# Performance work log

Hardware: AMD Instinct MI355X
Metric: run time of the kernel (lower is better)

## Reference

```python
import jax, jax.numpy as jnp
import numpy as np
from jax import lax

B, L, DDYN, DSTAT, H = 512, 64, 16, 8, 512
N_BANK, C_CAND, K_TOP, N_PROTO = 50000, 1024, 16, 8
T_TARG, Q_QUANT = 2, 3
TEMP = 0.2


def _l2norm(x, eps=1e-12):
    # matches torch.nn.functional.normalize: x / max(||x||, eps)
    n = jnp.sqrt(jnp.sum(x * x, axis=-1, keepdims=True))
    return x / jnp.maximum(n, eps)


def setup_inputs() -> dict:
    key = jax.random.key(0)
    ks = jax.random.split(key, 24)
    s = 0.02
    inp = {
        'sequence_values': jax.random.normal(ks[0], (B, L, DDYN), jnp.float32),
        'sequence_masks': jnp.ones((B, L), jnp.float32),
        'static_values': jax.random.normal(ks[1], (B, DSTAT), jnp.float32),
        'bank_keys': jax.random.normal(ks[2], (N_BANK, H), jnp.float32),
        'bank_values': jax.random.normal(ks[3], (N_BANK, H), jnp.float32),
        'candidate_indices': jax.random.randint(ks[4], (B, C_CAND), 0, N_BANK, jnp.int64),
        # encoder params (SequenceEncoder stand-in: masked-mean + linear + relu)
        'W_seq': jax.random.normal(ks[5], (DDYN, H), jnp.float32) * s,
        'W_stat': jax.random.normal(ks[6], (DSTAT, H), jnp.float32) * s,
        'b_enc': jnp.zeros((H,), jnp.float32),
        # retrieval / prototype / fusion params
        'W_q': jax.random.normal(ks[7], (H, H), jnp.float32) * s,
        'b_q': jnp.zeros((H,), jnp.float32),
        'prototype_tokens': jax.random.normal(ks[8], (N_PROTO, H), jnp.float32) * 0.02,
        'W_tr': jax.random.normal(ks[9], (2 * H, H), jnp.float32) * s,
        'b_tr': jnp.zeros((H,), jnp.float32),
        'W_gate': jax.random.normal(ks[10], (3 * H, H), jnp.float32) * s,
        'b_gate': jnp.zeros((H,), jnp.float32),
        'W_out': jax.random.normal(ks[11], (H, H), jnp.float32) * s,
        'b_out': jnp.zeros((H,), jnp.float32),
        # per-target heads stacked: [T, H, Q] and [T, H]
        'W_quant': jax.random.normal(ks[12], (T_TARG, H, Q_QUANT), jnp.float32) * s,
        'b_quant': jnp.zeros((T_TARG, Q_QUANT), jnp.float32),
        'W_ev': jax.random.normal(ks[13], (T_TARG, H), jnp.float32) * s,
        'b_ev': jnp.zeros((T_TARG,), jnp.float32),
    }
    return inp


def reference(sequence_values, sequence_masks, static_values, bank_keys, bank_values,
              candidate_indices, W_seq, W_stat, b_enc, W_q, b_q, prototype_tokens,
              W_tr, b_tr, W_gate, b_gate, W_out, b_out, W_quant, b_quant, W_ev, b_ev):
    # --- encoder (masked mean pool + linear + relu stand-in for SequenceEncoder) ---
    m = sequence_masks[..., None]                                   # [B,L,1]
    pooled = (sequence_values * m).sum(1) / jnp.maximum(m.sum(1), 1e-6)
    local_hidden = jax.nn.relu(pooled @ W_seq + static_values @ W_stat + b_enc)  # [B,H]

    # --- normalized query ---
    query = _l2norm(local_hidden @ W_q + b_q)                       # [B,H]

    # --- donor retrieval: gather + dot + topk + softmax + weighted sum ---
    cand_keys = bank_keys[candidate_indices]                        # [B,C,H]
    sim = jnp.einsum('bch,bh->bc', cand_keys, query)                # [B,C]
    top_scores, top_pos = lax.top_k(sim, K_TOP)                     # [B,K]
    weights = jax.nn.softmax(top_scores / max(TEMP, 1e-6), axis=-1)
    sel_idx = jnp.take_along_axis(candidate_indices, top_pos, axis=1)  # [B,K]
    donor_hidden = jnp.einsum('bk,bkh->bh', weights, bank_values[sel_idx])

    # --- prototype attention ---
    protos_n = _l2norm(prototype_tokens)                            # [P,H]
    pw = jax.nn.softmax(query @ protos_n.T, axis=-1)                # [B,P]
    proto_hidden = pw @ prototype_tokens                            # [B,H]

    # --- transfer / gate / fuse (dropout is identity at eval) ---
    transfer = jax.nn.relu(jnp.concatenate([donor_hidden, proto_hidden], -1) @ W_tr + b_tr)
    gate = jax.nn.sigmoid(
        jnp.concatenate([local_hidden, donor_hidden, proto_hidden], -1) @ W_gate + b_gate)
    fused = gate * local_hidden + (1.0 - gate) * transfer
    fused = jax.nn.relu(fused @ W_out + b_out)                      # [B,H]

    # --- heads: sorted quantiles [B,T,Q] and event logits [B,T] ---
    quant = jnp.sort(jnp.einsum('bh,thq->btq', fused, W_quant) + b_quant, axis=-1)
    logit = jnp.einsum('bh,th->bt', fused, W_ev) + b_ev
    return jnp.concatenate([quant.reshape(quant.shape[0], -1), logit], axis=-1)  # [B, T*Q+T]
```

## Files before the change

### kernel.cpp

```cpp
#include <hip/hip_runtime.h>
#include <hip/hip_bf16.h>

typedef __hip_bfloat16 bf16;
typedef float f4v __attribute__((ext_vector_type(4)));
typedef float f2v __attribute__((ext_vector_type(2)));

__device__ __forceinline__ float lo16(unsigned u){ return __uint_as_float(u << 16); }
__device__ __forceinline__ float hi16(unsigned u){ return __uint_as_float(u & 0xffff0000u); }

#define Bn 512
#define Hn 512
#define Cn 1024
#define Kn 16
#define NBANK 50000
#define NIDPAD 50176

__device__ __forceinline__ int clamp_id(int id){
    return (id < 0) ? 0 : ((id >= NBANK) ? (NBANK - 1) : id);
}

#define A_OFF    0
#define B_OFF    262144
#define C_OFF    524288
#define D_OFF    786432
#define SIM_OFF  1048576
#define ELO_OFF  1048576
#define EHI_OFF  1310720
#define F_OFF    1572864
#define G_OFF2   1835008
#define WS_FLOATS 2097152

#define HIST_I   0
#define CURSOR_I NIDPAD
#define GTOT_I   (2*NIDPAD)
#define OFFS_I   (2*NIDPAD + 256)

__global__ __launch_bounds__(256) void k_enc(
    const float* __restrict__ seq, const float* __restrict__ mask, const float* __restrict__ stat,
    const float* __restrict__ W_seq, const float* __restrict__ W_stat, const float* __restrict__ b_enc,
    const int* __restrict__ cand32, float* __restrict__ ws)
{
    const int b = blockIdx.x, t = threadIdx.x;
    const int h0 = 2*t, h1 = 2*t + 1;

    {
        const int c64 = ((cand32[1] | cand32[3] | cand32[5] | cand32[7]) == 0) ? 1 : 0;
        int* hist = (int*)(ws + F_OFF) + HIST_I;
        #pragma unroll
        for (int u = 0; u < 4; u++) {
            int idx = b*Cn + u*256 + t;
            atomicAdd(&hist[clamp_id(cand32[(size_t)idx << c64])], 1);
        }
    }

    __shared__ float s_pool[16], s_stat[8];
    if (t < 16) {
        float acc = 0.f, ms = 0.f;
        for (int l = 0; l < 64; l++) {
            float m = mask[b*64 + l];
            ms  += m;
            acc += seq[(b*64 + l)*16 + t] * m;
        }
        s_pool[t] = acc / fmaxf(ms, 1e-6f);
    } else if (t < 24) {
        s_stat[t - 16] = stat[b*8 + (t - 16)];
    }
    __syncthreads();
    float a0 = b_enc[h0], a1 = b_enc[h1];
    #pragma unroll
    for (int j = 0; j < 16; j++) {
        float2 wv = *(const float2*)(W_seq + j*Hn + h0);
        a0 += s_pool[j]*wv.x; a1 += s_pool[j]*wv.y;
    }
    #pragma unroll
    for (int j = 0; j < 8; j++) {
        float2 wv = *(const float2*)(W_stat + j*Hn + h0);
        a0 += s_stat[j]*wv.x; a1 += s_stat[j]*wv.y;
    }
    float* g = ws + B_OFF + (size_t)b*Hn;
    g[h0] = fmaxf(a0, 0.f); g[h1] = fmaxf(a1, 0.f);
}

__global__ __launch_bounds__(256) void k_scan(
    const int* __restrict__ hist, int* __restrict__ offs, int* __restrict__ gtot)
{
    __shared__ int s[256]; __shared__ int sbase;
    const int t = threadIdx.x, g = blockIdx.x*256 + t;
    const int v = hist[g];
    s[t] = v; __syncthreads();
    #pragma unroll
    for (int off = 1; off < 256; off <<= 1) {
        int x = (t >= off) ? s[t - off] : 0;
        __syncthreads();
        s[t] += x;
        __syncthreads();
    }
    if (t == 255) sbase = atomicAdd(gtot, s[255]);
    __syncthreads();
    offs[g] = sbase + s[t] - v;
}

__global__ __launch_bounds__(256) void k_scatter(
    const int* __restrict__ cand32, int* __restrict__ cursor,
    const int* __restrict__ offs, unsigned* __restrict__ refs)
{
    const int i = blockIdx.x*256 + threadIdx.x;
    const int c64 = ((cand32[1] | cand32[3] | cand32[5] | cand32[7]) == 0) ? 1 : 0;
    const int id = clamp_id(cand32[(size_t)i << c64]);
    const int pos = atomicAdd(&cursor[id], 1);
    refs[offs[id] + pos] = (unsigned)i;
}

__global__ __launch_bounds__(256) void k_qgemm_p(
    const float* __restrict__ W, const float* __restrict__ bias,
    const float* __restrict__ in,
    float* __restrict__ P0, float* __restrict__ P1,
    float* __restrict__ P2, float* __restrict__ P3)
{
    const int ct = blockIdx.x, rt = blockIdx.y, kz = blockIdx.z, t = threadIdx.x;
    __shared__ float lt[64][132];
    {
        int r = t >> 2, c0 = (t & 3)*32;
        const float* src = in + (size_t)(rt*64 + r)*Hn + kz*128 + c0;
        #pragma unroll
        for (int i = 0; i < 8; i++)
            *(float4*)&lt[r][c0 + i*4] = *(const float4*)(src + i*4);
    }
    __syncthreads();
    const int col0 = ct*64 + (t & 15)*4, rbase = (t >> 4)*4;
    float acc[4][4];
    if (kz == 0) {
        float4 bv = *(const float4*)(bias + col0);
        #pragma unroll
        for (int i = 0; i < 4; i++) { acc[i][0]=bv.x; acc[i][1]=bv.y; acc[i][2]=bv.z; acc[i][3]=bv.w; }
    } else {
        #pragma unroll
        for (int i = 0; i < 4; i++) { acc[i][0]=0; acc[i][1]=0; acc[i][2]=0; acc[i][3]=0; }
    }
    const float* wp = W + (size_t)(kz*128)*Hn + col0;
    #pragma unroll 4
    for (int k = 0; k < 128; k++) {
        float4 wv = *(const float4*)(wp + (size_t)k*Hn);
        #pragma unroll
        for (int i = 0; i < 4; i++) {
            float a = lt[rbase + i][k];
            acc[i][0] += a*wv.x; acc[i][1] += a*wv.y; acc[i][2] += a*wv.z; acc[i][3] += a*wv.w;
        }
    }
    float* outp = (kz == 0) ? P0 : (kz == 1) ? P1 : (kz == 2) ? P2 : P3;
    #pragma unroll
    for (int i = 0; i < 4; i++) {
        float* op = outp + (size_t)(rt*64 + rbase + i)*Hn + col0;
        *(float4*)op = make_float4(acc[i][0], acc[i][1], acc[i][2], acc[i][3]);
    }
}

__global__ __launch_bounds__(256) void k_qnorm(float* __restrict__ ws)
{
    const int b = blockIdx.x*4 + (threadIdx.x >> 6), lane = threadIdx.x & 63;
    const size_t o = (size_t)b*Hn + lane*8;
    const float* p0 = ws + A_OFF   + o;
    const float* p1 = ws + ELO_OFF + o;
    const float* p2 = ws + EHI_OFF + o;
    const float* p3 = ws + G_OFF2  + o;
    float4 qa, qb;
    {
        float4 a0 = *(const float4*)p0, a1 = *(const float4*)p1,
               a2 = *(const float4*)p2, a3 = *(const float4*)p3;
        qa = make_float4(((a0.x+a1.x)+a2.x)+a3.x, ((a0.y+a1.y)+a2.y)+a3.y,
                         ((a0.z+a1.z)+a2.z)+a3.z, ((a0.w+a1.w)+a2.w)+a3.w);
        float4 b0 = *(const float4*)(p0+4), b1 = *(const float4*)(p1+4),
               b2 = *(const float4*)(p2+4), b3 = *(const float4*)(p3+4);
        qb = make_float4(((b0.x+b1.x)+b2.x)+b3.x, ((b0.y+b1.y)+b2.y)+b3.y,
                         ((b0.z+b1.z)+b2.z)+b3.z, ((b0.w+b1.w)+b2.w)+b3.w);
    }
    float ss = qa.x*qa.x + qa.y*qa.y + qa.z*qa.z + qa.w*qa.w
             + qb.x*qb.x + qb.y*qb.y + qb.z*qb.z + qb.w*qb.w;
    #pragma unroll
    for (int o2 = 32; o2; o2 >>= 1) ss += __shfl_xor(ss, o2);
    float inv = 1.f / fmaxf(sqrtf(ss), 1e-12f);
    qa.x *= inv; qa.y *= inv; qa.z *= inv; qa.w *= inv;
    qb.x *= inv; qb.y *= inv; qb.z *= inv; qb.w *= inv;
    float* qr = ws + A_OFF + o;
    *(float4*)qr = qa; *(float4*)(qr + 4) = qb;
}

#define DI_LOAD(R0,R1,R2,R3,A0,Bq0,A1,Bq1,A2,Bq2,A3,Bq3,BASE) do {                       \
    int j0_=(BASE), j1_=(BASE)+1, j2_=(BASE)+2, j3_=(BASE)+3;                            \
    const int m_ = n - 1;                                                                \
    const int c1_ = (j1_ < n), c2_ = (j2_ < n), c3_ = (j3_ < n);                         \
    j0_ = j0_>m_?m_:j0_; j1_ = j1_>m_?m_:j1_; j2_ = j2_>m_?m_:j2_; j3_ = j3_>m_?m_:j3_;  \
    R0 = (j0_<64)?(unsigned)__shfl((int)refv,j0_):__builtin_nontemporal_load(refs+start+j0_); \
    R1 = (j1_<64)?(unsigned)__shfl((int)refv,j1_):__builtin_nontemporal_load(refs+start+j1_); \
    R2 = (j2_<64)?(unsigned)__shfl((int)refv,j2_):__builtin_nontemporal_load(refs+start+j2_); \
    R3 = (j3_<64)?(unsigned)__shfl((int)refv,j3_):__builtin_nontemporal_load(refs+start+j3_); \
    {   const float* q0_ = qbase + (size_t)(R0>>10)*Hn + lane*8;                         \
        A0 = *(const float4*)q0_; Bq0 = *(const float4*)(q0_+4); }                       \
    if (c1_) { const float* q1_ = qbase + (size_t)(R1>>10)*Hn + lane*8;                  \
        A1 = *(const float4*)q1_; Bq1 = *(const float4*)(q1_+4); }                       \
    if (c2_) { const float* q2_ = qbase + (size_t)(R2>>10)*Hn + lane*8;                  \
        A2 = *(const float4*)q2_; Bq2 = *(const float4*)(q2_+4); }                       \
    if (c3_) { const float* q3_ = qbase + (size_t)(R3>>10)*Hn + lane*8;                  \
        A3 = *(const float4*)q3_; Bq3 = *(const float4*)(q3_+4); }                       \
} while(0)

#define DI_COMP(R0,R1,R2,R3,A0,Bq0,A1,Bq1,A2,Bq2,A3,Bq3,BASE) do {                       \
    float s0_ = ka.x*A0.x + ka.y*A0.y + ka.z*A0.z + ka.w*A0.w                            \
              + kb.x*Bq0.x + kb.y*Bq0.y + kb.z*Bq0.z + kb.w*Bq0.w;                       \
    float s1_ = ka.x*A1.x + ka.y*A1.y + ka.z*A1.z + ka.w*A1.w                            \
              + kb.x*Bq1.x + kb.y*Bq1.y + kb.z*Bq1.z + kb.w*Bq1.w;                       \
    float s2_ = ka.x*A2.x + ka.y*A2.y + ka.z*A2.z + ka.w*A2.w                            \
              + kb.x*Bq2.x + kb.y*Bq2.y + kb.z*Bq2.z + kb.w*Bq2.w;                       \
    float s3_ = ka.x*A3.x + ka.y*A3.y + ka.z*A3.z + ka.w*A3.w                            \
              + kb.x*Bq3.x + kb.y*Bq3.y + kb.z*Bq3.z + kb.w*Bq3.w;                       \
    s0_ += __shfl_xor(s0_,32); s1_ += __shfl_xor(s1_,32);                                \
    s2_ += __shfl_xor(s2_,32); s3_ += __shfl_xor(s3_,32);                                \
    s0_ += __shfl_xor(s0_,16); s1_ += __shfl_xor(s1_,16);                                \
    s2_ += __shfl_xor(s2_,16); s3_ += __shfl_xor(s3_,16);                                \
    s0_ += __shfl_xor(s0_, 8); s1_ += __shfl_xor(s1_, 8);                                \
    s2_ += __shfl_xor(s2_, 8); s3_ += __shfl_xor(s3_, 8);                                \
    int d_ = (lane >> 3) & 3;                                                            \
    float t_ = d_==0 ? s0_ : d_==1 ? s1_ : d_==2 ? s2_ : s3_;                            \
    t_ += __shfl_xor(t_, 4); t_ += __shfl_xor(t_, 2); t_ += __shfl_xor(t_, 1);           \
    if ((lane & 7) == 0 && lane < 32) {                                                  \
        int dd_ = lane >> 3;                                                             \
        if ((BASE) + dd_ < n) {                                                          \
            unsigned rs_ = dd_==0 ? R0 : dd_==1 ? R1 : dd_==2 ? R2 : R3;                 \
            simw[rs_] = t_;                                                              \
        }                                                                                \
    }                                                                                    \
} while(0)

__global__ __launch_bounds__(256) void k_dotinv(
    const float* __restrict__ bank_keys, const unsigned* __restrict__ refs,
    const int* __restrict__ offs, const int* __restrict__ cnt,
    float* __restrict__ ws)
{
    const int id = blockIdx.x*4 + (threadIdx.x >> 6);
    const int lane = threadIdx.x & 63;
    const int n = cnt[id];
    if (n <= 0) return;
    const int start = offs[id];

    const float* kp = bank_keys + (size_t)id*Hn + lane*8;
    f4v kav = __builtin_nontemporal_load((const f4v*)kp);
    f4v kbv = __builtin_nontemporal_load((const f4v*)(kp + 4));
    float4 ka = make_float4(kav.x, kav.y, kav.z, kav.w);
    float4 kb = make_float4(kbv.x, kbv.y, kbv.z, kbv.w);
    const unsigned refv = refs[start + (lane < n ? lane : n - 1)];
    const float* qbase = ws + A_OFF;
    float* simw = ws + SIM_OFF;

    unsigned Ar0,Ar1,Ar2,Ar3, Br0=0,Br1=0,Br2=0,Br3=0;
    float4 Aa0,Ab0,Aa1,Ab1,Aa2,Ab2,Aa3,Ab3;
    float4 Ba0,Bb0,Ba1,Bb1,Ba2,Bb2,Ba3,Bb3;
    Aa0=Ab0=Aa1=Ab1=Aa2=Ab2=Aa3=Ab3=make_float4(0.f,0.f,0.f,0.f);
    Ba0=Bb0=Ba1=Bb1=Ba2=Bb2=Ba3=Bb3=make_float4(0.f,0.f,0.f,0.f);

    DI_LOAD(Ar0,Ar1,Ar2,Ar3, Aa0,Ab0,Aa1,Ab1,Aa2,Ab2,Aa3,Ab3, 0);
    for (int base = 0; ; ) {
        if (base + 4 < n) DI_LOAD(Br0,Br1,Br2,Br3, Ba0,Bb0,Ba1,Bb1,Ba2,Bb2,Ba3,Bb3, base + 4);
        DI_COMP(Ar0,Ar1,Ar2,Ar3, Aa0,Ab0,Aa1,Ab1,Aa2,Ab2,Aa3,Ab3, base);
        if (base + 8 < n) DI_LOAD(Ar0,Ar1,Ar2,Ar3, Aa0,Ab0,Aa1,Ab1,Aa2,Ab2,Aa3,Ab3, base + 8);
        DI_COMP(Br0,Br1,Br2,Br3, Ba0,Bb0,Ba1,Bb1,Ba2,Bb2,Ba3,Bb3, base + 4);
        base += 8;
        if (base >= n) break;
    }
}

__global__ __launch_bounds__(256) void k_select(
    const float* __restrict__ bank_values, const int* __restrict__ cand32,
    const float* __restrict__ proto, float* __restrict__ ws)
{
    const int b = blockIdx.x, t = threadIdx.x;
    const int w = t >> 6, lane = t & 63;
    const int h0 = 2*t, h1 = 2*t + 1;
    const int c64 = ((cand32[1] | cand32[3] | cand32[5] | cand32[7]) == 0) ? 1 : 0;

    __shared__ __align__(16) float s_sim[Cn];
    __shared__ float s_bv[4]; __shared__ int s_bi[4];
    __shared__ float s_topv[Kn]; __shared__ int s_sel[Kn];
    __shared__ float s_w[Kn];
    __shared__ float s_score[8], s_pw[8];

    *(float4*)&s_sim[t*4] = *(const float4*)(ws + SIM_OFF + (size_t)b*Cn + t*4);

    const float* qr = ws + A_OFF + (size_t)b*Hn + lane*8;
    float4 qa = *(const float4*)qr, qb = *(const float4*)(qr + 4);
    float qv[8] = {qa.x, qa.y, qa.z, qa.w, qb.x, qb.y, qb.z, qb.w};
    __syncthreads();

    for (int k = 0; k < Kn; k++) {
        float best = -1e30f; int bi = 0x7fffffff;
        for (int i = t; i < Cn; i += 256) {
            float v = s_sim[i];
            if (v > best || (v == best && i < bi)) { best = v; bi = i; }
        }
        #pragma unroll
        for (int o = 32; o; o >>= 1) {
            float ov = __shfl_xor(best, o); int oi = __shfl_xor(bi, o);
            if (ov > best || (ov == best && oi < bi)) { best = ov; bi = oi; }
        }
        if (lane == 0) { s_bv[w] = best; s_bi[w] = bi; }
        __syncthreads();
        if (t == 0) {
            float bv = s_bv[0]; int bbi = s_bi[0];
            for (int x = 1; x < 4; x++)
                if (s_bv[x] > bv || (s_bv[x] == bv && s_bi[x] < bbi)) { bv = s_bv[x]; bbi = s_bi[x]; }
            if (bbi < 0 || bbi >= Cn) bbi = 0;
            s_topv[k] = bv; s_sel[k] = bbi; s_sim[bbi] = -1e30f;
        }
        __syncthreads();
    }

    if (t == 0) {
        float m = s_topv[0];
        float e[Kn], ssum = 0.f;
        for (int k = 0; k < Kn; k++) { e[k] = __expf((s_topv[k] - m) * 5.0f); ssum += e[k]; }
        float inv = 1.f / ssum;
        for (int k = 0; k < Kn; k++) s_w[k] = e[k] * inv;
    }
    for (int p = w; p < 8; p += 4) {
        const float* pp = proto + (size_t)p*Hn + lane*8;
        float4 pa = *(const float4*)pp, pb = *(const float4*)(pp + 4);
        float f[8] = {pa.x, pa.y, pa.z, pa.w, pb.x, pb.y, pb.z, pb.w};
        float dq = 0.f, sq = 0.f;
        #pragma unroll
        for (int i = 0; i < 8; i++) { dq += f[i]*qv[i]; sq += f[i]*f[i]; }
        #pragma unroll
        for (int o = 32; o; o >>= 1) { dq += __shfl_xor(dq, o); sq += __shfl_xor(sq, o); }
        if (lane == 0) s_score[p] = dq / fmaxf(sqrtf(sq), 1e-12f);
    }
    __syncthreads();
    if (t == 0) {
        float m = s_score[0];
        for (int p = 1; p < 8; p++) m = fmaxf(m, s_score[p]);
        float e[8], ssum = 0.f;
        for (int p = 0; p < 8; p++) { e[p] = __expf(s_score[p] - m); ssum += e[p]; }
        float inv = 1.f / ssum;
        for (int p = 0; p < 8; p++) s_pw[p] = e[p] * inv;
    }
    __syncthreads();

    {
        float a0 = 0.f, a1 = 0.f;
        #pragma unroll
        for (int k = 0; k < Kn; k++) {
            int id = clamp_id(cand32[(size_t)(b*Cn + s_sel[k]) << c64]);
            f2v v = __builtin_nontemporal_load((const f2v*)(bank_values + (size_t)id*Hn + h0));
            a0 += s_w[k]*v.x; a1 += s_w[k]*v.y;
        }
        float* gd = ws + C_OFF + (size_t)b*Hn;
        gd[h0] = a0; gd[h1] = a1;
    }
    {
        float a0 = 0.f, a1 = 0.f;
        #pragma unroll
        for (int p = 0; p < 8; p++) {
            float2 v = *(const float2*)(proto + (size_t)p*Hn + h0);
            a0 += s_pw[p]*v.x; a1 += s_pw[p]*v.y;
        }
        float* gp = ws + D_OFF + (size_t)b*Hn;
        gp[h0] = a0; gp[h1] = a1;
    }
}

__global__ __launch_bounds__(256) void k_gatetr_p(
    const float* __restrict__ W_tr, const float* __restrict__ b_tr,
    const float* __restrict__ W_gate, const float* __restrict__ b_gate,
    float* __restrict__ ws)
{
    const int ct = blockIdx.x, rt = blockIdx.y, z = blockIdx.z, t = threadIdx.x;
    const int isGate = (z < 3);
    const int sl = isGate ? z : (z - 3);
    const float* W = isGate ? (W_gate + (size_t)(z*512)*Hn) : (W_tr + (size_t)(sl*512)*Hn);
    const float* slab = ws + B_OFF + (size_t)(isGate ? z : (sl + 1))*262144;
    float* outp = isGate
        ? ((z == 0) ? ws + A_OFF : (z == 1) ? ws + ELO_OFF : ws + EHI_OFF)
        : ((sl == 0) ? ws + F_OFF : ws + G_OFF2);

    __shared__ float lt[32][260];
    const int col0 = ct*128 + (t & 31)*4, rbase = (t >> 5)*4;
    float acc[4][4];
    if (z == 0 || z == 3) {
        const float* bias = isGate ? b_gate : b_tr;
        float4 bv = *(const float4*)(bias + col0);
        #pragma unroll
        for (int i = 0; i < 4; i++) { acc[i][0]=bv.x; acc[i][1]=bv.y; acc[i][2]=bv.z; acc[i][3]=bv.w; }
    } else {
        #pragma unroll
        for (int i = 0; i < 4; i++) { acc[i][0]=0; acc[i][1]=0; acc[i][2]=0; acc[i][3]=0; }
    }

    #pragma unroll
    for (int h = 0; h < 2; h++) {
        if (h) __syncthreads();
        {
            int r = t >> 3, c0 = (t & 7)*32;
            const float* src = slab + (size_t)(rt*32 + r)*Hn + h*256 + c0;
            #pragma unroll
            for (int i = 0; i < 8; i++)
                *(float4*)&lt[r][c0 + i*4] = *(const float4*)(src + i*4);
        }
        __syncthreads();
        const float* wp = W + (size_t)(h*256)*Hn + col0;
        #pragma unroll 4
        for (int k = 0; k < 256; k++) {
            float4 wv = *(const float4*)(wp + (size_t)k*Hn);
            #pragma unroll
            for (int i = 0; i < 4; i++) {
                float a = lt[rbase + i][k];
                acc[i][0] += a*wv.x; acc[i][1] += a*wv.y; acc[i][2] += a*wv.z; acc[i][3] += a*wv.w;
            }
        }
    }
    #pragma unroll
    for (int i = 0; i < 4; i++) {
        float* op = outp + (size_t)(rt*32 + rbase + i)*Hn + col0;
        *(float4*)op = make_float4(acc[i][0], acc[i][1], acc[i][2], acc[i][3]);
    }
}

__global__ __launch_bounds__(256) void k_f1ew(float* __restrict__ ws)
{
    const int i4 = blockIdx.x*256 + threadIdx.x;
    const size_t off = (size_t)(i4 >> 7)*Hn + (i4 & 127)*4;
    float4 lc = *(const float4*)(ws + B_OFF + off);
    float4 g0 = *(const float4*)(ws + A_OFF + off);
    float4 g1 = *(const float4*)(ws + ELO_OFF + off);
    float4 g2 = *(const float4*)(ws + EHI_OFF + off);
    float4 t0 = *(const float4*)(ws + F_OFF + off);
    float4 t1 = *(const float4*)(ws + G_OFF2 + off);
    float4 ga = make_float4((g0.x+g1.x)+g2.x, (g0.y+g1.y)+g2.y,
                            (g0.z+g1.z)+g2.z, (g0.w+g1.w)+g2.w);
    float4 tr = make_float4(t0.x+t1.x, t0.y+t1.y, t0.z+t1.z, t0.w+t1.w);
    float4 r;
    float s;
    s = 1.f/(1.f + __expf(-ga.x)); r.x = s*lc.x + (1.f-s)*fmaxf(tr.x, 0.f);
    s = 1.f/(1.f + __expf(-ga.y)); r.y = s*lc.y + (1.f-s)*fmaxf(tr.y, 0.f);
    s = 1.f/(1.f + __expf(-ga.z)); r.z = s*lc.z + (1.f-s)*fmaxf(tr.z, 0.f);
    s = 1.f/(1.f + __expf(-ga.w)); r.w = s*lc.w + (1.f-s)*fmaxf(tr.w, 0.f);
    *(float4*)(ws + A_OFF + off) = r;
}

__global__ __launch_bounds__(64) void k_heads(
    const float* __restrict__ W_quant, const float* __restrict__ b_quant,
    const float* __restrict__ W_ev, const float* __restrict__ b_ev,
    const float* __restrict__ ws_ro, float* __restrict__ out)
{
    const int b = blockIdx.x, lane = threadIdx.x;
    const size_t o = (size_t)b*Hn + lane*8;
    const float* p0 = ws_ro + ELO_OFF + o;
    const float* p1 = ws_ro + EHI_OFF + o;
    const float* p2 = ws_ro + F_OFF + o;
    const float* p3 = ws_ro + G_OFF2 + o;
    float4 a0 = *(const float4*)p0, a1 = *(const float4*)p1,
           a2 = *(const float4*)p2, a3 = *(const float4*)p3;
    float4 b0 = *(const float4*)(p0+4), b1 = *(const float4*)(p1+4),
           b2 = *(const float4*)(p2+4), b3 = *(const float4*)(p3+4);
    float fv[8] = {
        fmaxf(((a0.x+a1.x)+a2.x)+a3.x, 0.f), fmaxf(((a0.y+a1.y)+a2.y)+a3.y, 0.f),
        fmaxf(((a0.z+a1.z)+a2.z)+a3.z, 0.f), fmaxf(((a0.w+a1.w)+a2.w)+a3.w, 0.f),
        fmaxf(((b0.x+b1.x)+b2.x)+b3.x, 0.f), fmaxf(((b0.y+b1.y)+b2.y)+b3.y, 0.f),
        fmaxf(((b0.z+b1.z)+b2.z)+b3.z, 0.f), fmaxf(((b0.w+b1.w)+b2.w)+b3.w, 0.f)};
    float acc[8];
    #pragma unroll
    for (int q = 0; q < 8; q++) acc[q] = 0.f;
    #pragma unroll
    for (int i = 0; i < 8; i++) {
        int h = lane*8 + i;
        float fh = fv[i];
        acc[0] += fh*W_quant[(0*Hn + h)*3 + 0];
        acc[1] += fh*W_quant[(0*Hn + h)*3 + 1];
        acc[2] += fh*W_quant[(0*Hn + h)*3 + 2];
        acc[3] += fh*W_quant[(1*Hn + h)*3 + 0];
        acc[4] += fh*W_quant[(1*Hn + h)*3 + 1];
        acc[5] += fh*W_quant[(1*Hn + h)*3 + 2];
        acc[6] += fh*W_ev[0*Hn + h];
        acc[7] += fh*W_ev[1*Hn + h];
    }
    #pragma unroll
    for (int q = 0; q < 8; q++) {
        #pragma unroll
        for (int s = 32; s; s >>= 1) acc[q] += __shfl_xor(acc[q], s);
    }
    if (lane == 0) {
        float qv[6];
        for (int q = 0; q < 6; q++) qv[q] = acc[q] + b_quant[q];
        #pragma unroll
        for (int tt = 0; tt < 2; tt++) {
            float a = qv[tt*3], bb = qv[tt*3+1], c = qv[tt*3+2];
            float mn = fminf(a, fminf(bb, c)), mx = fmaxf(a, fmaxf(bb, c));
            float md = a + bb + c - mn - mx;
            qv[tt*3] = mn; qv[tt*3+1] = md; qv[tt*3+2] = mx;
        }
        for (int q = 0; q < 6; q++) out[b*8 + q] = qv[q];
        out[b*8 + 6] = acc[6] + b_ev[0];
        out[b*8 + 7] = acc[7] + b_ev[1];
    }
}

__device__ __forceinline__ float lds_f(const void* p, int i, int f32){
    return f32 ? ((const float*)p)[i] : __bfloat162float(((const bf16*)p)[i]);
}
__device__ __forceinline__ float2 ldpair(const void* p, int elt, int f32){
    if (f32) return ((const float2*)p)[elt >> 1];
    unsigned u = ((const unsigned*)p)[elt >> 1];
    return make_float2(lo16(u), hi16(u));
}
__device__ __forceinline__ void ld8(const void* p, int elt, int f32, float* v){
    if (f32){
        const float4* q = (const float4*)((const float*)p + elt);
        float4 a = q[0], b = q[1];
        v[0]=a.x; v[1]=a.y; v[2]=a.z; v[3]=a.w; v[4]=b.x; v[5]=b.y; v[6]=b.z; v[7]=b.w;
    } else {
        uint4 u = *(const uint4*)((const bf16*)p + elt);
        v[0]=lo16(u.x); v[1]=hi16(u.x); v[2]=lo16(u.y); v[3]=hi16(u.y);
        v[4]=lo16(u.z); v[5]=hi16(u.z); v[6]=lo16(u.w); v[7]=hi16(u.w);
    }
}
__device__ __forceinline__ void st_out(void* o, int i, int f32, float v){
    if (f32) ((float*)o)[i] = v; else ((bf16*)o)[i] = __float2bfloat16(v);
}

__global__ __launch_bounds__(256) void k_fused(
    const void* __restrict__ seq, const void* __restrict__ mask, const void* __restrict__ stat,
    const void* __restrict__ bank_keys, const void* __restrict__ bank_values,
    const int* __restrict__ cand32,
    const void* __restrict__ W_seq, const void* __restrict__ W_stat, const void* __restrict__ b_enc,
    const void* __restrict__ W_q, const void* __restrict__ b_q,
    const void* __restrict__ proto,
    const void* __restrict__ W_tr, const void* __restrict__ b_tr,
    const void* __restrict__ W_gate, const void* __restrict__ b_gate,
    const void* __restrict__ W_out, const void* __restrict__ b_out,
    const void* __restrict__ W_quant, const void* __restrict__ b_quant,
    const void* __restrict__ W_ev, const void* __restrict__ b_ev,
    void* __restrict__ out)
{
    const int b = blockIdx.x, t = threadIdx.x;
    const int w = t >> 6, lane = t & 63;
    const int h0 = 2*t, h1 = 2*t + 1;
    const int f32 = (((const unsigned short*)mask)[0] == 0) ? 1 : 0;
    const int c64 = ((cand32[1] | cand32[3] | cand32[5] | cand32[7]) == 0) ? 1 : 0;

    __shared__ __align__(16) float s_pool[16];
    __shared__ __align__(16) float s_stat[8];
    __shared__ __align__(16) float g[1536];
    __shared__ __align__(16) float s_q[Hn];
    __shared__ __align__(16) float s_sim[Cn];
    __shared__ __align__(16) float f1[Hn];
    __shared__ __align__(16) float f2[Hn];
    __shared__ float s_part[4], s_ss;
// ... 188 lines not shown
            acc[6] += fh*lds_f(W_ev, 0*Hn + h, f32);
            acc[7] += fh*lds_f(W_ev, 1*Hn + h, f32);
        }
        #pragma unroll
        for (int o = 0; o < 8; o++) {
            float v = acc[o];
            #pragma unroll
            for (int s = 32; s; s >>= 1) v += __shfl_xor(v, s);
            if (lane == 0) s_head[o][w] = v;
        }
        __syncthreads();
        if (t == 0) {
            float q[6];
            for (int o = 0; o < 6; o++)
                q[o] = s_head[o][0] + s_head[o][1] + s_head[o][2] + s_head[o][3] + lds_f(b_quant, o, f32);
            #pragma unroll
            for (int tt = 0; tt < 2; tt++) {
                float a = q[tt*3], bb = q[tt*3+1], c = q[tt*3+2];
                float mn = fminf(a, fminf(bb, c)), mx = fmaxf(a, fmaxf(bb, c));
                float md = a + bb + c - mn - mx;
                q[tt*3] = mn; q[tt*3+1] = md; q[tt*3+2] = mx;
            }
            for (int o = 0; o < 6; o++) st_out(out, b*8 + o, f32, q[o]);
            float l0 = s_head[6][0] + s_head[6][1] + s_head[6][2] + s_head[6][3] + lds_f(b_ev, 0, f32);
            float l1 = s_head[7][0] + s_head[7][1] + s_head[7][2] + s_head[7][3] + lds_f(b_ev, 1, f32);
            st_out(out, b*8 + 6, f32, l0);
            st_out(out, b*8 + 7, f32, l1);
        }
    }
}

extern "C" void kernel_launch(void* const* d_in, const int* in_sizes, int n_in,
                              void* d_out, int out_size, void* d_ws, size_t ws_size,
                              hipStream_t stream) {
    static const int expect[22] = {
        512*64*16, 512*64, 512*8, 50000*512, 50000*512, 512*1024,
        16*512, 8*512, 512, 512*512, 512, 8*512,
        1024*512, 512, 1536*512, 512, 512*512, 512,
        2*512*3, 2*3, 2*512, 2
    };
    if (n_in != 22 || out_size != 512*8) return;
    for (int i = 0; i < 22; i++) if (in_sizes[i] != expect[i]) return;

    if (ws_size < (size_t)WS_FLOATS * 4) {
        k_fused<<<Bn, 256, 0, stream>>>(
            d_in[0], d_in[1], d_in[2], d_in[3], d_in[4], (const int*)d_in[5],
            d_in[6], d_in[7], d_in[8], d_in[9], d_in[10], d_in[11],
            d_in[12], d_in[13], d_in[14], d_in[15], d_in[16], d_in[17],
            d_in[18], d_in[19], d_in[20], d_in[21], d_out);
        return;
    }

    float* ws = (float*)d_ws;
    int* iws = (int*)(ws + F_OFF);
    int* hist   = iws + HIST_I;
    int* cursor = iws + CURSOR_I;
    int* gtot   = iws + GTOT_I;
    int* offs   = iws + OFFS_I;
    unsigned* refs = (unsigned*)(ws + C_OFF);

    hipMemsetAsync(iws, 0, (size_t)(2*NIDPAD + 256)*4, stream);

    k_enc<<<Bn, 256, 0, stream>>>((const float*)d_in[0], (const float*)d_in[1],
                                  (const float*)d_in[2], (const float*)d_in[6],
                                  (const float*)d_in[7], (const float*)d_in[8],
                                  (const int*)d_in[5], ws);
    k_scan<<<NIDPAD/256, 256, 0, stream>>>(hist, offs, gtot);
    k_scatter<<<(Bn*Cn)/256, 256, 0, stream>>>((const int*)d_in[5], cursor, offs, refs);
    k_qgemm_p<<<dim3(8, 8, 4), 256, 0, stream>>>(
        (const float*)d_in[9], (const float*)d_in[10], ws + B_OFF,
        ws + A_OFF, ws + ELO_OFF, ws + EHI_OFF, ws + G_OFF2);
    k_qnorm<<<Bn/4, 256, 0, stream>>>(ws);
    k_dotinv<<<NBANK/4, 256, 0, stream>>>((const float*)d_in[3], refs, offs, hist, ws);
    k_select<<<Bn, 256, 0, stream>>>((const float*)d_in[4], (const int*)d_in[5],
                                     (const float*)d_in[11], ws);
    k_gatetr_p<<<dim3(4, 16, 5), 256, 0, stream>>>(
        (const float*)d_in[12], (const float*)d_in[13],
        (const float*)d_in[14], (const float*)d_in[15], ws);
    k_f1ew<<<256, 256, 0, stream>>>(ws);
    k_qgemm_p<<<dim3(8, 8, 4), 256, 0, stream>>>(
        (const float*)d_in[16], (const float*)d_in[17], ws + A_OFF,
        ws + ELO_OFF, ws + EHI_OFF, ws + F_OFF, ws + G_OFF2);
    k_heads<<<Bn, 64, 0, stream>>>((const float*)d_in[18], (const float*)d_in[19],
                                   (const float*)d_in[20], (const float*)d_in[21],
                                   ws, (float*)d_out);
}
```

Before: 500.4 us.

## Merge the kernel chain into two cooperative persistent kernels with grid syncs

The stage kernels are turned into device functions and called from two cooperative persistent kernels. Inside each kernel the stages are separated by grid.sync, and blocks loop over the work items, replacing about eleven launches plus a memset with two launches. The intent is to cut launch overhead and the idle gaps between the many small stages. The cost is a grid-wide barrier per stage and lower parallelism for stages that used to launch many blocks, such as dotinv with 12500 blocks. The old multi-launch path is kept as a fallback.

```diff
diff --git a/kernel.cpp b/kernel.cpp
--- a/kernel.cpp
+++ b/kernel.cpp
@@ -1,5 +1,8 @@
 #include <hip/hip_runtime.h>
 #include <hip/hip_bf16.h>
+#include <hip/hip_cooperative_groups.h>
+
+namespace cg = cooperative_groups;
 
 typedef __hip_bfloat16 bf16;
 typedef float f4v __attribute__((ext_vector_type(4)));
@@ -31,29 +34,23 @@
 #define WS_FLOATS 2097152
 
 #define HIST_I   0
-#define CURSOR_I NIDPAD
-#define GTOT_I   (2*NIDPAD)
+#define GTOT_I   NIDPAD
+#define CURSOR_I (NIDPAD + 256)
 #define OFFS_I   (2*NIDPAD + 256)
 
-__global__ __launch_bounds__(256) void k_enc(
-    const float* __restrict__ seq, const float* __restrict__ mask, const float* __restrict__ stat,
-    const float* __restrict__ W_seq, const float* __restrict__ W_stat, const float* __restrict__ b_enc,
-    const int* __restrict__ cand32, float* __restrict__ ws)
-{
-    const int b = blockIdx.x, t = threadIdx.x;
-    const int h0 = 2*t, h1 = 2*t + 1;
-
-    {
-        const int c64 = ((cand32[1] | cand32[3] | cand32[5] | cand32[7]) == 0) ? 1 : 0;
-        int* hist = (int*)(ws + F_OFF) + HIST_I;
-        #pragma unroll
-        for (int u = 0; u < 4; u++) {
-            int idx = b*Cn + u*256 + t;
-            atomicAdd(&hist[clamp_id(cand32[(size_t)idx << c64])], 1);
-        }
-    }
-
-    __shared__ float s_pool[16], s_stat[8];
+
+__device__ __forceinline__ void enc_body(
+    int b, int t, const float* __restrict__ seq, const float* __restrict__ mask,
+    const float* __restrict__ stat, const float* __restrict__ W_seq,
+    const float* __restrict__ W_stat, const float* __restrict__ b_enc,
+    const int* __restrict__ cand32, int c64, int* __restrict__ hist,
+    float* __restrict__ ws, float* s_pool, float* s_stat)
+{
+    #pragma unroll
+    for (int u = 0; u < 4; u++) {
+        int idx = b*Cn + u*256 + t;
+        atomicAdd(&hist[clamp_id(cand32[(size_t)idx << c64])], 1);
+    }
     if (t < 16) {
         float acc = 0.f, ms = 0.f;
         for (int l = 0; l < 64; l++) {
@@ -66,6 +63,7 @@
         s_stat[t - 16] = stat[b*8 + (t - 16)];
     }
     __syncthreads();
+    const int h0 = 2*t, h1 = 2*t + 1;
     float a0 = b_enc[h0], a1 = b_enc[h1];
     #pragma unroll
     for (int j = 0; j < 16; j++) {
@@ -81,13 +79,14 @@
     g[h0] = fmaxf(a0, 0.f); g[h1] = fmaxf(a1, 0.f);
 }
 
-__global__ __launch_bounds__(256) void k_scan(
-    const int* __restrict__ hist, int* __restrict__ offs, int* __restrict__ gtot)
-{
-    __shared__ int s[256]; __shared__ int sbase;
-    const int t = threadIdx.x, g = blockIdx.x*256 + t;
-    const int v = hist[g];
-    s[t] = v; __syncthreads();
+__device__ __forceinline__ void scan_body(
+    int v, int t, const int* __restrict__ hist, int* __restrict__ offs,
+    int* __restrict__ gtot, int* __restrict__ cursor, int* s )
+{
+    const int g = v*256 + t;
+    const int val = hist[g];
+    cursor[g] = 0;
+    s[t] = val; __syncthreads();
     #pragma unroll
     for (int off = 1; off < 256; off <<= 1) {
         int x = (t >= off) ? s[t - off] : 0;
@@ -95,30 +94,28 @@
         s[t] += x;
         __syncthreads();
     }
-    if (t == 255) sbase = atomicAdd(gtot, s[255]);
-    __syncthreads();
-    offs[g] = sbase + s[t] - v;
-}
-
-__global__ __launch_bounds__(256) void k_scatter(
-    const int* __restrict__ cand32, int* __restrict__ cursor,
+    if (t == 255) s[256] = atomicAdd(gtot, s[255]);
+    __syncthreads();
+    offs[g] = s[256] + s[t] - val;
+}
+
+__device__ __forceinline__ void scatter_body(
+    int i, int c64, const int* __restrict__ cand32, int* __restrict__ cursor,
     const int* __restrict__ offs, unsigned* __restrict__ refs)
 {
-    const int i = blockIdx.x*256 + threadIdx.x;
-    const int c64 = ((cand32[1] | cand32[3] | cand32[5] | cand32[7]) == 0) ? 1 : 0;
     const int id = clamp_id(cand32[(size_t)i << c64]);
     const int pos = atomicAdd(&cursor[id], 1);
     refs[offs[id] + pos] = (unsigned)i;
 }
 
-__global__ __launch_bounds__(256) void k_qgemm_p(
+__device__ __forceinline__ void qgemm_body(
+    int ct, int rt, int kz, int t,
     const float* __restrict__ W, const float* __restrict__ bias,
     const float* __restrict__ in,
     float* __restrict__ P0, float* __restrict__ P1,
-    float* __restrict__ P2, float* __restrict__ P3)
-{
-    const int ct = blockIdx.x, rt = blockIdx.y, kz = blockIdx.z, t = threadIdx.x;
-    __shared__ float lt[64][132];
+    float* __restrict__ P2, float* __restrict__ P3,
+    float (*lt)[132])
+{
     {
         int r = t >> 2, c0 = (t & 3)*32;
         const float* src = in + (size_t)(rt*64 + r)*Hn + kz*128 + c0;
@@ -155,9 +152,8 @@
     }
 }
 
-__global__ __launch_bounds__(256) void k_qnorm(float* __restrict__ ws)
-{
-    const int b = blockIdx.x*4 + (threadIdx.x >> 6), lane = threadIdx.x & 63;
+__device__ __forceinline__ void qnorm_body(int b, int lane, float* __restrict__ ws)
+{
     const size_t o = (size_t)b*Hn + lane*8;
     const float* p0 = ws + A_OFF   + o;
     const float* p1 = ws + ELO_OFF + o;
@@ -231,13 +227,12 @@
     }                                                                                    \
 } while(0)
 
-__global__ __launch_bounds__(256) void k_dotinv(
-    const float* __restrict__ bank_keys, const unsigned* __restrict__ refs,
-    const int* __restrict__ offs, const int* __restrict__ cnt,
-    float* __restrict__ ws)
-{
-    const int id = blockIdx.x*4 + (threadIdx.x >> 6);
-    const int lane = threadIdx.x & 63;
+__device__ __forceinline__ void dotinv_wave(
+    int id, int lane, const float* __restrict__ bank_keys,
+    const unsigned* __restrict__ refs, const int* __restrict__ offs,
+    const int* __restrict__ cnt, const float* __restrict__ qbase,
+    float* __restrict__ simw)
+{
     const int n = cnt[id];
     if (n <= 0) return;
     const int start = offs[id];
@@ -248,8 +243,6 @@
     float4 ka = make_float4(kav.x, kav.y, kav.z, kav.w);
     float4 kb = make_float4(kbv.x, kbv.y, kbv.z, kbv.w);
     const unsigned refv = refs[start + (lane < n ? lane : n - 1)];
-    const float* qbase = ws + A_OFF;
-    float* simw = ws + SIM_OFF;
 
     unsigned Ar0,Ar1,Ar2,Ar3, Br0=0,Br1=0,Br2=0,Br3=0;
     float4 Aa0,Ab0,Aa1,Ab1,Aa2,Ab2,Aa3,Ab3;
@@ -268,22 +261,23 @@
     }
 }
 
-__global__ __launch_bounds__(256) void k_select(
-    const float* __restrict__ bank_values, const int* __restrict__ cand32,
-    const float* __restrict__ proto, float* __restrict__ ws)
-{
-    const int b = blockIdx.x, t = threadIdx.x;
+struct SelS {
+    float s_sim[Cn];
+    float s_bv[4]; int s_bi[4];
+    float s_topv[Kn]; int s_sel[Kn];
+    float s_w[Kn];
+    float s_score[8], s_pw[8];
+};
+
+__device__ __forceinline__ void select_body(
+    int b, int t, const float* __restrict__ bank_values,
+    const int* __restrict__ cand32, int c64, const float* __restrict__ proto,
+    float* __restrict__ ws, SelS* S)
+{
     const int w = t >> 6, lane = t & 63;
     const int h0 = 2*t, h1 = 2*t + 1;
-    const int c64 = ((cand32[1] | cand32[3] | cand32[5] | cand32[7]) == 0) ? 1 : 0;
-
-    __shared__ __align__(16) float s_sim[Cn];
-    __shared__ float s_bv[4]; __shared__ int s_bi[4];
-    __shared__ float s_topv[Kn]; __shared__ int s_sel[Kn];
-    __shared__ float s_w[Kn];
-    __shared__ float s_score[8], s_pw[8];
-
-    *(float4*)&s_sim[t*4] = *(const float4*)(ws + SIM_OFF + (size_t)b*Cn + t*4);
+
+    *(float4*)&S->s_sim[t*4] = *(const float4*)(ws + SIM_OFF + (size_t)b*Cn + t*4);
 
     const float* qr = ws + A_OFF + (size_t)b*Hn + lane*8;
     float4 qa = *(const float4*)qr, qb = *(const float4*)(qr + 4);
@@ -293,7 +287,7 @@
     for (int k = 0; k < Kn; k++) {
         float best = -1e30f; int bi = 0x7fffffff;
         for (int i = t; i < Cn; i += 256) {
-            float v = s_sim[i];
+            float v = S->s_sim[i];
             if (v > best || (v == best && i < bi)) { best = v; bi = i; }
         }
         #pragma unroll
@@ -301,24 +295,24 @@
             float ov = __shfl_xor(best, o); int oi = __shfl_xor(bi, o);
             if (ov > best || (ov == best && oi < bi)) { best = ov; bi = oi; }
         }
-        if (lane == 0) { s_bv[w] = best; s_bi[w] = bi; }
+        if (lane == 0) { S->s_bv[w] = best; S->s_bi[w] = bi; }
         __syncthreads();
         if (t == 0) {
-            float bv = s_bv[0]; int bbi = s_bi[0];
+            float bv = S->s_bv[0]; int bbi = S->s_bi[0];
             for (int x = 1; x < 4; x++)
-                if (s_bv[x] > bv || (s_bv[x] == bv && s_bi[x] < bbi)) { bv = s_bv[x]; bbi = s_bi[x]; }
+                if (S->s_bv[x] > bv || (S->s_bv[x] == bv && S->s_bi[x] < bbi)) { bv = S->s_bv[x]; bbi = S->s_bi[x]; }
             if (bbi < 0 || bbi >= Cn) bbi = 0;
-            s_topv[k] = bv; s_sel[k] = bbi; s_sim[bbi] = -1e30f;
+            S->s_topv[k] = bv; S->s_sel[k] = bbi; S->s_sim[bbi] = -1e30f;
         }
         __syncthreads();
     }
 
     if (t == 0) {
-        float m = s_topv[0];
+        float m = S->s_topv[0];
         float e[Kn], ssum = 0.f;
-        for (int k = 0; k < Kn; k++) { e[k] = __expf((s_topv[k] - m) * 5.0f); ssum += e[k]; }
+        for (int k = 0; k < Kn; k++) { e[k] = __expf((S->s_topv[k] - m) * 5.0f); ssum += e[k]; }
         float inv = 1.f / ssum;
-        for (int k = 0; k < Kn; k++) s_w[k] = e[k] * inv;
+        for (int k = 0; k < Kn; k++) S->s_w[k] = e[k] * inv;
     }
     for (int p = w; p < 8; p += 4) {
         const float* pp = proto + (size_t)p*Hn + lane*8;
@@ -329,16 +323,16 @@
         for (int i = 0; i < 8; i++) { dq += f[i]*qv[i]; sq += f[i]*f[i]; }
         #pragma unroll
         for (int o = 32; o; o >>= 1) { dq += __shfl_xor(dq, o); sq += __shfl_xor(sq, o); }
-        if (lane == 0) s_score[p] = dq / fmaxf(sqrtf(sq), 1e-12f);
+        if (lane == 0) S->s_score[p] = dq / fmaxf(sqrtf(sq), 1e-12f);
     }
     __syncthreads();
     if (t == 0) {
-        float m = s_score[0];
-        for (int p = 1; p < 8; p++) m = fmaxf(m, s_score[p]);
+        float m = S->s_score[0];
+        for (int p = 1; p < 8; p++) m = fmaxf(m, S->s_score[p]);
         float e[8], ssum = 0.f;
-        for (int p = 0; p < 8; p++) { e[p] = __expf(s_score[p] - m); ssum += e[p]; }
+        for (int p = 0; p < 8; p++) { e[p] = __expf(S->s_score[p] - m); ssum += e[p]; }
         float inv = 1.f / ssum;
-        for (int p = 0; p < 8; p++) s_pw[p] = e[p] * inv;
+        for (int p = 0; p < 8; p++) S->s_pw[p] = e[p] * inv;
     }
     __syncthreads();
 
@@ -346,9 +340,9 @@
         float a0 = 0.f, a1 = 0.f;
         #pragma unroll
         for (int k = 0; k < Kn; k++) {
-            int id = clamp_id(cand32[(size_t)(b*Cn + s_sel[k]) << c64]);
+            int id = clamp_id(cand32[(size_t)(b*Cn + S->s_sel[k]) << c64]);
             f2v v = __builtin_nontemporal_load((const f2v*)(bank_values + (size_t)id*Hn + h0));
-            a0 += s_w[k]*v.x; a1 += s_w[k]*v.y;
+            a0 += S->s_w[k]*v.x; a1 += S->s_w[k]*v.y;
         }
         float* gd = ws + C_OFF + (size_t)b*Hn;
         gd[h0] = a0; gd[h1] = a1;
@@ -358,19 +352,19 @@
         #pragma unroll
         for (int p = 0; p < 8; p++) {
             float2 v = *(const float2*)(proto + (size_t)p*Hn + h0);
-            a0 += s_pw[p]*v.x; a1 += s_pw[p]*v.y;
+            a0 += S->s_pw[p]*v.x; a1 += S->s_pw[p]*v.y;
         }
         float* gp = ws + D_OFF + (size_t)b*Hn;
         gp[h0] = a0; gp[h1] = a1;
     }
 }
 
-__global__ __launch_bounds__(256) void k_gatetr_p(
+__device__ __forceinline__ void gatetr_body(
+    int ct, int rt, int z, int t,
     const float* __restrict__ W_tr, const float* __restrict__ b_tr,
     const float* __restrict__ W_gate, const float* __restrict__ b_gate,
-    float* __restrict__ ws)
-{
-    const int ct = blockIdx.x, rt = blockIdx.y, z = blockIdx.z, t = threadIdx.x;
+    float* __restrict__ ws, float (*lt)[260])
+{
     const int isGate = (z < 3);
     const int sl = isGate ? z : (z - 3);
     const float* W = isGate ? (W_gate + (size_t)(z*512)*Hn) : (W_tr + (size_t)(sl*512)*Hn);
@@ -379,7 +373,6 @@
         ? ((z == 0) ? ws + A_OFF : (z == 1) ? ws + ELO_OFF : ws + EHI_OFF)
         : ((sl == 0) ? ws + F_OFF : ws + G_OFF2);
 
-    __shared__ float lt[32][260];
     const int col0 = ct*128 + (t & 31)*4, rbase = (t >> 5)*4;
     float acc[4][4];
     if (z == 0 || z == 3) {
@@ -421,9 +414,8 @@
     }
 }
 
-__global__ __launch_bounds__(256) void k_f1ew(float* __restrict__ ws)
-{
-    const int i4 = blockIdx.x*256 + threadIdx.x;
+__device__ __forceinline__ void f1ew_body(int i4, float* __restrict__ ws)
+{
     const size_t off = (size_t)(i4 >> 7)*Hn + (i4 & 127)*4;
     float4 lc = *(const float4*)(ws + B_OFF + off);
     float4 g0 = *(const float4*)(ws + A_OFF + off);
@@ -443,12 +435,11 @@
     *(float4*)(ws + A_OFF + off) = r;
 }
 
-__global__ __launch_bounds__(64) void k_heads(
-    const float* __restrict__ W_quant, const float* __restrict__ b_quant,
+__device__ __forceinline__ void heads_body(
+    int b, int lane, const float* __restrict__ W_quant, const float* __restrict__ b_quant,
     const float* __restrict__ W_ev, const float* __restrict__ b_ev,
     const float* __restrict__ ws_ro, float* __restrict__ out)
 {
-    const int b = blockIdx.x, lane = threadIdx.x;
     const size_t o = (size_t)b*Hn + lane*8;
     const float* p0 = ws_ro + ELO_OFF + o;
     const float* p1 = ws_ro + EHI_OFF + o;
@@ -498,6 +489,210 @@
         out[b*8 + 6] = acc[6] + b_ev[0];
         out[b*8 + 7] = acc[7] + b_ev[1];
     }
+}
+
+
+#define COOP_SMEM 33792
+
+__global__ __launch_bounds__(256, 4) void k_coopA(
+    const float* __restrict__ seq, const float* __restrict__ mask, const float* __restrict__ stat,
+    const float* __restrict__ W_seq, const float* __restrict__ W_stat, const float* __restrict__ b_enc,
+    const int* __restrict__ cand32, const float* __restrict__ W_q, const float* __restrict__ b_q,
+    const float* __restrict__ bank_keys, float* __restrict__ ws)
+{
+    cg::grid_group grid = cg::this_grid();
+    const int bid = blockIdx.x, nb = gridDim.x, t = threadIdx.x;
+    __shared__ __align__(16) char smem[COOP_SMEM];
+
+    int* iws = (int*)(ws + F_OFF);
+    int* hist   = iws + HIST_I;
+    int* gtot   = iws + GTOT_I;
+    int* cursor = iws + CURSOR_I;
+    int* offs   = iws + OFFS_I;
+    unsigned* refs = (unsigned*)(ws + C_OFF);
+    const int c64 = ((cand32[1] | cand32[3] | cand32[5] | cand32[7]) == 0) ? 1 : 0;
+
+    for (int i = bid*256 + t; i < NIDPAD + 256; i += nb*256) hist[i] = 0;
+    grid.sync();
+
+    {
+        float* s_pool = (float*)smem;
+        float* s_stat = (float*)(smem + 64);
+        for (int b = bid; b < Bn; b += nb) {
+            enc_body(b, t, seq, mask, stat, W_seq, W_stat, b_enc, cand32, c64, hist, ws, s_pool, s_stat);
+            __syncthreads();
+        }
+    }
+    grid.sync();
+
+    {
+        float (*lt)[132] = (float(*)[132])smem;
+        for (int v = bid; v < 256; v += nb) {
+            qgemm_body(v & 7, (v >> 3) & 7, v >> 6, t, W_q, b_q, ws + B_OFF,
+                       ws + A_OFF, ws + ELO_OFF, ws + EHI_OFF, ws + G_OFF2, lt);
+            __syncthreads();
+        }
+    }
+    grid.sync();
+
+    {
+        int* s_scan = (int*)smem;
+        for (int v = bid; v < 324; v += nb) {
+            if (v < 196) scan_body(v, t, hist, offs, gtot, cursor, s_scan);
+            else         qnorm_body((v - 196)*4 + (t >> 6), t & 63, ws);
+            __syncthreads();
+        }
+    }
+    grid.sync();
+
+    for (int v = bid; v < 2048; v += nb) {
+        scatter_body(v*256 + t, c64, cand32, cursor, offs, refs);
+    }
+    grid.sync();
+
+    {
+        const float* qbase = ws + A_OFF;
+        float* simw = ws + SIM_OFF;
+        const int lane = t & 63;
+        for (int v = bid; v < 12500; v += nb) {
+            dotinv_wave(v*4 + (t >> 6), lane, bank_keys, refs, offs, hist, qbase, simw);
+        }
+    }
+}
+
+__global__ __launch_bounds__(256, 4) void k_coopB(
+    const float* __restrict__ bank_values, const int* __restrict__ cand32,
+    const float* __restrict__ proto,
+    const float* __restrict__ W_tr, const float* __restrict__ b_tr,
+    const float* __restrict__ W_gate, const float* __restrict__ b_gate,
+    const float* __restrict__ W_out, const float* __restrict__ b_out,
+    const float* __restrict__ W_quant, const float* __restrict__ b_quant,
+    const float* __restrict__ W_ev, const float* __restrict__ b_ev,
+    float* __restrict__ ws, float* __restrict__ out)
+{
+    cg::grid_group grid = cg::this_grid();
+    const int bid = blockIdx.x, nb = gridDim.x, t = threadIdx.x;
+    __shared__ __align__(16) char smem[COOP_SMEM];
+    const int c64 = ((cand32[1] | cand32[3] | cand32[5] | cand32[7]) == 0) ? 1 : 0;
+
+    {
+        SelS* S = (SelS*)smem;
+        for (int b = bid; b < Bn; b += nb) {
+            select_body(b, t, bank_values, cand32, c64, proto, ws, S);
+            __syncthreads();
+        }
+    }
+    grid.sync();
+
+    {
+        float (*lt)[260] = (float(*)[260])smem;
+        for (int v = bid; v < 320; v += nb) {
+            gatetr_body(v & 3, (v >> 2) & 15, v >> 6, t, W_tr, b_tr, W_gate, b_gate, ws, lt);
+            __syncthreads();
+        }
+    }
+    grid.sync();
+
+    for (int i4 = bid*256 + t; i4 < 65536; i4 += nb*256) f1ew_body(i4, ws);
+    grid.sync();
+
+    {
+        float (*lt)[132] = (float(*)[132])smem;
+        for (int v = bid; v < 256; v += nb) {
+            qgemm_body(v & 7, (v >> 3) & 7, v >> 6, t, W_out, b_out, ws + A_OFF,
+                       ws + ELO_OFF, ws + EHI_OFF, ws + F_OFF, ws + G_OFF2, lt);
+            __syncthreads();
+        }
+    }
+    grid.sync();
+
+    for (int b = bid; b < Bn; b += nb) {
+        if (t < 64) heads_body(b, t, W_quant, b_quant, W_ev, b_ev, ws, out);
+    }
+}
+
+
+__global__ __launch_bounds__(256) void k_enc(
+    const float* __restrict__ seq, const float* __restrict__ mask, const float* __restrict__ stat,
+    const float* __restrict__ W_seq, const float* __restrict__ W_stat, const float* __restrict__ b_enc,
+    const int* __restrict__ cand32, float* __restrict__ ws)
+{
+    __shared__ float s_pool[16], s_stat[8];
+    const int c64 = ((cand32[1] | cand32[3] | cand32[5] | cand32[7]) == 0) ? 1 : 0;
+    int* hist = (int*)(ws + F_OFF) + HIST_I;
+    enc_body(blockIdx.x, threadIdx.x, seq, mask, stat, W_seq, W_stat, b_enc,
+             cand32, c64, hist, ws, s_pool, s_stat);
+}
+
+__global__ __launch_bounds__(256) void k_scan(
+    const int* __restrict__ hist, int* __restrict__ offs, int* __restrict__ gtot,
+    int* __restrict__ cursor)
+{
+    __shared__ int s[257];
+    scan_body(blockIdx.x, threadIdx.x, hist, offs, gtot, cursor, s);
+}
+
+__global__ __launch_bounds__(256) void k_scatter(
+    const int* __restrict__ cand32, int* __restrict__ cursor,
+    const int* __restrict__ offs, unsigned* __restrict__ refs)
+{
+    const int c64 = ((cand32[1] | cand32[3] | cand32[5] | cand32[7]) == 0) ? 1 : 0;
+    scatter_body(blockIdx.x*256 + threadIdx.x, c64, cand32, cursor, offs, refs);
+}
+
+__global__ __launch_bounds__(256) void k_qgemm_p(
+    const float* __restrict__ W, const float* __restrict__ bias,
+    const float* __restrict__ in,
+    float* __restrict__ P0, float* __restrict__ P1,
+    float* __restrict__ P2, float* __restrict__ P3)
+{
+    __shared__ float lt[64][132];
+    qgemm_body(blockIdx.x, blockIdx.y, blockIdx.z, threadIdx.x, W, bias, in, P0, P1, P2, P3, lt);
+}
+
+__global__ __launch_bounds__(256) void k_qnorm(float* __restrict__ ws)
+{
+    qnorm_body(blockIdx.x*4 + (threadIdx.x >> 6), threadIdx.x & 63, ws);
+}
+
+__global__ __launch_bounds__(256) void k_dotinv(
+    const float* __restrict__ bank_keys, const unsigned* __restrict__ refs,
+    const int* __restrict__ offs, const int* __restrict__ cnt,
+    float* __restrict__ ws)
+{
+    dotinv_wave(blockIdx.x*4 + (threadIdx.x >> 6), threadIdx.x & 63,
+                bank_keys, refs, offs, cnt, ws + A_OFF, ws + SIM_OFF);
+}
+
+__global__ __launch_bounds__(256) void k_select(
+    const float* __restrict__ bank_values, const int* __restrict__ cand32,
+    const float* __restrict__ proto, float* __restrict__ ws)
+{
+    __shared__ SelS S;
+    const int c64 = ((cand32[1] | cand32[3] | cand32[5] | cand32[7]) == 0) ? 1 : 0;
+    select_body(blockIdx.x, threadIdx.x, bank_values, cand32, c64, proto, ws, &S);
+}
+
+__global__ __launch_bounds__(256) void k_gatetr_p(
+    const float* __restrict__ W_tr, const float* __restrict__ b_tr,
+    const float* __restrict__ W_gate, const float* __restrict__ b_gate,
+    float* __restrict__ ws)
+{
+    __shared__ float lt[32][260];
+    gatetr_body(blockIdx.x, blockIdx.y, blockIdx.z, threadIdx.x, W_tr, b_tr, W_gate, b_gate, ws, lt);
+}
+
+__global__ __launch_bounds__(256) void k_f1ew(float* __restrict__ ws)
+{
+    f1ew_body(blockIdx.x*256 + threadIdx.x, ws);
+}
+
+__global__ __launch_bounds__(64) void k_heads(
+    const float* __restrict__ W_quant, const float* __restrict__ b_quant,
+    const float* __restrict__ W_ev, const float* __restrict__ b_ev,
+    const float* __restrict__ ws_ro, float* __restrict__ out)
+{
+    heads_body(blockIdx.x, threadIdx.x, W_quant, b_quant, W_ev, b_ev, ws_ro, out);
 }
 
 __device__ __forceinline__ float lds_f(const void* p, int i, int f32){
@@ -792,36 +987,77 @@
     }
 
     float* ws = (float*)d_ws;
+    const float* a_seq  = (const float*)d_in[0];
+    const float* a_mask = (const float*)d_in[1];
+    const float* a_stat = (const float*)d_in[2];
+    const float* a_bk   = (const float*)d_in[3];
+    const float* a_bv   = (const float*)d_in[4];
+    const int*   a_cand = (const int*)d_in[5];
+    const float* a_Wseq = (const float*)d_in[6];
+    const float* a_Wstat= (const float*)d_in[7];
+    const float* a_benc = (const float*)d_in[8];
+    const float* a_Wq   = (const float*)d_in[9];
+    const float* a_bq   = (const float*)d_in[10];
+    const float* a_proto= (const float*)d_in[11];
+    const float* a_Wtr  = (const float*)d_in[12];
+    const float* a_btr  = (const float*)d_in[13];
+    const float* a_Wg   = (const float*)d_in[14];
+    const float* a_bg   = (const float*)d_in[15];
+    const float* a_Wout = (const float*)d_in[16];
+    const float* a_bout = (const float*)d_in[17];
+    const float* a_Wqu  = (const float*)d_in[18];
+    const float* a_bqu  = (const float*)d_in[19];
+    const float* a_Wev  = (const float*)d_in[20];
+    const float* a_bev  = (const float*)d_in[21];
+    float* a_out = (float*)d_out;
+
+    int ncu = 0, occA = 0, occB = 0;
+    int dev = 0;
+    bool coop_ok = (hipGetDevice(&dev) == hipSuccess) &&
+        (hipDeviceGetAttribute(&ncu, hipDeviceAttributeMultiprocessorCount, dev) == hipSuccess) &&
+        (hipOccupancyMaxActiveBlocksPerMultiprocessor(&occA, k_coopA, 256, 0) == hipSuccess) &&
+        (hipOccupancyMaxActiveBlocksPerMultiprocessor(&occB, k_coopB, 256, 0) == hipSuccess) &&
+        (ncu >= 1) && (occA >= 1) && (occB >= 1);
+
+    if (coop_ok) {
+        int gA = occA * ncu; if (gA > 2048) gA = 2048;
+        int gB = occB * ncu; if (gB > 2048) gB = 2048;
+        void* argsA[] = { (void*)&a_seq, (void*)&a_mask, (void*)&a_stat,
+                          (void*)&a_Wseq, (void*)&a_Wstat, (void*)&a_benc,
+                          (void*)&a_cand, (void*)&a_Wq, (void*)&a_bq,
+                          (void*)&a_bk, (void*)&ws };
+        void* argsB[] = { (void*)&a_bv, (void*)&a_cand, (void*)&a_proto,
+                          (void*)&a_Wtr, (void*)&a_btr, (void*)&a_Wg, (void*)&a_bg,
+                          (void*)&a_Wout, (void*)&a_bout,
+                          (void*)&a_Wqu, (void*)&a_bqu, (void*)&a_Wev, (void*)&a_bev,
+                          (void*)&ws, (void*)&a_out };
+        hipError_t eA = hipLaunchCooperativeKernel(k_coopA, dim3(gA), dim3(256), argsA, 0, stream);
+        if (eA == hipSuccess) {
+            hipError_t eB = hipLaunchCooperativeKernel(k_coopB, dim3(gB), dim3(256), argsB, 0, stream);
+            if (eB == hipSuccess) return;
+        }
+    }
+
     int* iws = (int*)(ws + F_OFF);
     int* hist   = iws + HIST_I;
+    int* gtot   = iws + GTOT_I;
     int* cursor = iws + CURSOR_I;
-    int* gtot   = iws + GTOT_I;
     int* offs   = iws + OFFS_I;
     unsigned* refs = (unsigned*)(ws + C_OFF);
 
-    hipMemsetAsync(iws, 0, (size_t)(2*NIDPAD + 256)*4, stream);
-
-    k_enc<<<Bn, 256, 0, stream>>>((const float*)d_in[0], (const float*)d_in[1],
-                                  (const float*)d_in[2], (const float*)d_in[6],
-                                  (const float*)d_in[7], (const float*)d_in[8],
-                                  (const int*)d_in[5], ws);
-    k_scan<<<NIDPAD/256, 256, 0, stream>>>(hist, offs, gtot);
-    k_scatter<<<(Bn*Cn)/256, 256, 0, stream>>>((const int*)d_in[5], cursor, offs, refs);
+    hipMemsetAsync(iws, 0, (size_t)(NIDPAD + 256)*4, stream);
+
+    k_enc<<<Bn, 256, 0, stream>>>(a_seq, a_mask, a_stat, a_Wseq, a_Wstat, a_benc, a_cand, ws);
     k_qgemm_p<<<dim3(8, 8, 4), 256, 0, stream>>>(
-        (const float*)d_in[9], (const float*)d_in[10], ws + B_OFF,
-        ws + A_OFF, ws + ELO_OFF, ws + EHI_OFF, ws + G_OFF2);
+        a_Wq, a_bq, ws + B_OFF, ws + A_OFF, ws + ELO_OFF, ws + EHI_OFF, ws + G_OFF2);
     k_qnorm<<<Bn/4, 256, 0, stream>>>(ws);
-    k_dotinv<<<NBANK/4, 256, 0, stream>>>((const float*)d_in[3], refs, offs, hist, ws);
-    k_select<<<Bn, 256, 0, stream>>>((const float*)d_in[4], (const int*)d_in[5],
-                                     (const float*)d_in[11], ws);
-    k_gatetr_p<<<dim3(4, 16, 5), 256, 0, stream>>>(
-        (const float*)d_in[12], (const float*)d_in[13],
-        (const float*)d_in[14], (const float*)d_in[15], ws);
+    k_scan<<<NIDPAD/256, 256, 0, stream>>>(hist, offs, gtot, cursor);
+    k_scatter<<<(Bn*Cn)/256, 256, 0, stream>>>(a_cand, cursor, offs, refs);
+    k_dotinv<<<NBANK/4, 256, 0, stream>>>(a_bk, refs, offs, hist, ws);
+    k_select<<<Bn, 256, 0, stream>>>(a_bv, a_cand, a_proto, ws);
+    k_gatetr_p<<<dim3(4, 16, 5), 256, 0, stream>>>(a_Wtr, a_btr, a_Wg, a_bg, ws);
     k_f1ew<<<256, 256, 0, stream>>>(ws);
     k_qgemm_p<<<dim3(8, 8, 4), 256, 0, stream>>>(
-        (const float*)d_in[16], (const float*)d_in[17], ws + A_OFF,
-        ws + ELO_OFF, ws + EHI_OFF, ws + F_OFF, ws + G_OFF2);
-    k_heads<<<Bn, 64, 0, stream>>>((const float*)d_in[18], (const float*)d_in[19],
-                                   (const float*)d_in[20], (const float*)d_in[21],
-                                   ws, (float*)d_out);
-}
+        a_Wout, a_bout, ws + A_OFF, ws + ELO_OFF, ws + EHI_OFF, ws + F_OFF, ws + G_OFF2);
+    k_heads<<<Bn, 64, 0, stream>>>(a_Wqu, a_bqu, a_Wev, a_bev, ws, a_out);
+}
```

Result: slower. 1.065 ms (+112.9%).
